# Kernel optimization log

Measured on AMD Instinct MI355X. Metric: run time of the kernel, lower is better.

## Reference

```python
import jax, jax.numpy as jnp
import numpy as np

N_EMBD = 384
HEAD_SIZE = 64
B, T = 16, 2048


def setup_inputs() -> dict:
    key = jax.random.key(0)
    ks = jax.random.split(key, 7)
    s = 1.0 / np.sqrt(N_EMBD)
    return {
        "x": jax.random.normal(ks[0], (B, T, N_EMBD), dtype=jnp.float32),
        "Wq": jax.random.uniform(ks[1], (N_EMBD, HEAD_SIZE), jnp.float32, -s, s),
        "bq": jax.random.uniform(ks[2], (HEAD_SIZE,), jnp.float32, -s, s),
        "Wk": jax.random.uniform(ks[3], (N_EMBD, HEAD_SIZE), jnp.float32, -s, s),
        "bk": jax.random.uniform(ks[4], (HEAD_SIZE,), jnp.float32, -s, s),
        "Wv": jax.random.uniform(ks[5], (N_EMBD, HEAD_SIZE), jnp.float32, -s, s),
        "bv": jax.random.uniform(ks[6], (HEAD_SIZE,), jnp.float32, -s, s),
    }


def reference(x, Wq, bq, Wk, bk, Wv, bv):
    # QKV projections: [B,T,C] @ [C,H] -> [B,T,H]
    q = x @ Wq + bq
    k = x @ Wk + bk
    v = x @ Wv + bv
    scale = k.shape[-1] ** (-0.5)
    # NOTE: original forward applies NO causal mask (tril buffer unused).
    scores = jnp.einsum("bqh,bkh->bqk", q, k) * scale  # [B,T,T]
    wmap = jax.nn.softmax(scores, axis=-1)
    # dropout is identity in eval mode
    out = jnp.einsum("bqk,bkh->bqh", wmap, v)  # [B,T,H]
    return out
```

## Files before the change

kernel.cpp:

```cpp
#include <hip/hip_runtime.h>
#include <hip/hip_bf16.h>
#include <cstdint>

typedef unsigned short u16;
typedef __attribute__((ext_vector_type(8))) short short8;
typedef __attribute__((ext_vector_type(4))) short short4v;
typedef __attribute__((ext_vector_type(4))) float f32x4;

#define MFMA16(a, b, c) __builtin_amdgcn_mfma_f32_16x16x32_bf16((a), (b), (c), 0, 0, 0)

constexpr int Bn   = 16;
constexpr int Tn   = 2048;
constexpr int Cn   = 384;
constexpr int Hn   = 64;
constexpr int XPAD = 392;
constexpr int WPAD = 72;
constexpr long NTOK = (long)Bn * Tn;
constexpr long NELT = NTOK * Hn;

#define QSCALE 0.18033688011112042f

__device__ __forceinline__ u16 f2bf(float f) {
  union { float f; uint32_t u; } c; c.f = f;
  uint32_t u = c.u;
  return (u16)((u + 0x7fffu + ((u >> 16) & 1u)) >> 16);
}

__device__ __forceinline__ uint32_t pkbf(float a, float b) {
  uint32_t d;
  asm("v_cvt_pk_bf16_f32 %0, %1, %2" : "=v"(d) : "v"(a), "v"(b));
  return d;
}

__device__ __forceinline__ void gl16(const u16* g, const u16* l) {
  __builtin_amdgcn_global_load_lds(
      (const __attribute__((address_space(1))) void*)g,
      (__attribute__((address_space(3))) void*)l, 16, 0, 0);
}

__global__ __launch_bounds__(256) void qkv_proj(
    const float* __restrict__ x,
    const float* __restrict__ Wq, const float* __restrict__ bq,
    const float* __restrict__ Wk, const float* __restrict__ bk,
    const float* __restrict__ Wv, const float* __restrict__ bv,
    u16* __restrict__ oq, u16* __restrict__ ok, u16* __restrict__ ovt)
{
  __shared__ u16 xs[64 * XPAD];
  __shared__ u16 wt[3][Hn * WPAD];

  const int t    = threadIdx.x;
  const int lane = t & 63;
  const int w    = t >> 6;
  const int l15  = lane & 15;
  const int lh   = lane >> 4;
  const long r0  = (long)blockIdx.x * 64;

  #pragma unroll
  for (int i = 0; i < 24; ++i) {
    int f4  = t + i * 256;
    int row = f4 / 96, col4 = f4 % 96;
    const float4 xv = *reinterpret_cast<const float4*>(x + (r0 + row) * Cn + col4 * 4);
    u16* p = &xs[row * XPAD + col4 * 4];
    p[0] = f2bf(xv.x); p[1] = f2bf(xv.y); p[2] = f2bf(xv.z); p[3] = f2bf(xv.w);
  }

  const float* Ws[3] = {Wq, Wk, Wv};

  f32x4 acc[3][4];
  #pragma unroll
  for (int m = 0; m < 3; ++m)
    #pragma unroll
    for (int n = 0; n < 4; ++n) acc[m][n] = f32x4{0.f, 0.f, 0.f, 0.f};

  const int hh  = t & 63;
  const int kk0 = (t >> 6) * 16;

  for (int kc = 0; kc < 6; ++kc) {
    __syncthreads();
    #pragma unroll
    for (int m = 0; m < 3; ++m) {
      const float* Wp = Ws[m] + (size_t)(kc * 64 + kk0) * Hn + hh;
      union { short8 s; u16 u[8]; } p0, p1;
      #pragma unroll
      for (int j = 0; j < 8; ++j) p0.u[j] = f2bf(Wp[j * Hn]);
      #pragma unroll
      for (int j = 0; j < 8; ++j) p1.u[j] = f2bf(Wp[(8 + j) * Hn]);
      *reinterpret_cast<short8*>(&wt[m][hh * WPAD + kk0])     = p0.s;
      *reinterpret_cast<short8*>(&wt[m][hh * WPAD + kk0 + 8]) = p1.s;
    }
    __syncthreads();

    #pragma unroll
    for (int ks = 0; ks < 2; ++ks) {
      const short8 a = *reinterpret_cast<const short8*>(
          &xs[(w * 16 + l15) * XPAD + kc * 64 + ks * 32 + lh * 8]);
      #pragma unroll
      for (int m = 0; m < 3; ++m)
        #pragma unroll
        for (int n = 0; n < 4; ++n) {
          const short8 bfr = *reinterpret_cast<const short8*>(
              &wt[m][(n * 16 + l15) * WPAD + ks * 32 + lh * 8]);
          acc[m][n] = MFMA16(a, bfr, acc[m][n]);
        }
    }
  }

  {
    const float* bias[2] = {bq, bk};
    u16*         dst[2]  = {oq, ok};
    const float  scl[2]  = {QSCALE, 1.0f};
    #pragma unroll
    for (int m = 0; m < 2; ++m) {
      #pragma unroll
      for (int n = 0; n < 4; ++n) {
        int col = n * 16 + l15;
        float bb = bias[m][col];
        #pragma unroll
        for (int r = 0; r < 4; ++r) {
          int row = lh * 4 + r;
          dst[m][(r0 + w * 16 + row) * Hn + col] = f2bf((acc[m][n][r] + bb) * scl[m]);
        }
      }
    }
  }
  {
    const long g    = r0 + w * 16 + lh * 4;
    const long bidx = g >> 11;
    const long tloc = g & 2047;
    #pragma unroll
    for (int n = 0; n < 4; ++n) {
      int col = n * 16 + l15;
      float bb = bv[col];
      short4v pk;
      #pragma unroll
      for (int r = 0; r < 4; ++r) pk[r] = (short)f2bf(acc[2][n][r] + bb);
      *reinterpret_cast<short4v*>(ovt + (bidx * Hn + col) * Tn + tloc) = pk;
    }
  }
}

__global__ __launch_bounds__(256) void flash_attn(
    const u16* __restrict__ q, const u16* __restrict__ k,
    const u16* __restrict__ vt, float* __restrict__ opart,
    float* __restrict__ lpart)
{
  __shared__ u16 kbuf[2][64 * 64];
  __shared__ u16 vbuf[2][64 * 64];

  const int t    = threadIdx.x;
  const int lane = t & 63;
  const int w    = t >> 6;
  const int l15  = lane & 15;
  const int lh   = lane >> 4;
  const int swz_id = ((blockIdx.x & 7) << 7) | (blockIdx.x >> 3);
  const int qt    = swz_id & 31;
  const int split = (swz_id >> 5) & 1;
  const int b     = swz_id >> 6;
  const long rowbase = (long)b * Tn + qt * 64;
  const int it0 = split * 16, it1 = it0 + 16;

  short8 aq[2];
  {
    const u16* qrow = q + (rowbase + w * 16 + l15) * Hn;
    aq[0] = *reinterpret_cast<const short8*>(qrow + lh * 8);
    aq[1] = *reinterpret_cast<const short8*>(qrow + 32 + lh * 8);
  }

  f32x4 o[4];
  #pragma unroll
  for (int m = 0; m < 4; ++m) o[m] = f32x4{0.f, 0.f, 0.f, 0.f};
  float lacc = 0.f;

  const u16* kb_g = k  + (long)b * Tn * Hn;
  const u16* vb_g = vt + (long)b * Hn * Tn;

  const int g0 = t, g1 = 256 + t;
  const int r0g = g0 >> 3, c0g = g0 & 7;
  const int r1g = g1 >> 3, c1g = g1 & 7;
  const int ksrc0 = r0g * Hn + ((c0g ^ (r0g & 7)) << 3);
  const int ksrc1 = r1g * Hn + ((c1g ^ (r1g & 7)) << 3);
  const int wb0 = w * 64 * 8;
  const int wb1 = wb0 + 256 * 8;

  const int vrow = w * 16 + (lane >> 2);
  const int vc   = lane & 3;
  const long vgbase = (long)vrow * Tn + vc * 16;
  const int vs_ = vrow & 7;

  const int swz  = l15 & 7;
  const int cks0 = ((0 * 4 + lh) ^ swz) << 3;
  const int cks1 = ((1 * 4 + lh) ^ swz) << 3;
  const int rfr  = l15 * 64;

  int cur = 0;

  {
    const u16* kt = kb_g + (long)it0 * 64 * Hn;
    gl16(kt + ksrc0, &kbuf[0][wb0]);
    gl16(kt + ksrc1, &kbuf[0][wb1]);
    const short8 v0 = *reinterpret_cast<const short8*>(vb_g + vgbase + it0 * 64);
    const short8 v1 = *reinterpret_cast<const short8*>(vb_g + vgbase + it0 * 64 + 8);
    u16* vdst = &vbuf[0][0] + vrow * 64;
    const int gb = (vc >> 1) * 4, off8 = (vc & 1) * 4;
    *reinterpret_cast<short4v*>(vdst + (((gb + 0) ^ vs_) << 3) + off8) = short4v{v0[0], v0[1], v0[2], v0[3]};
    *reinterpret_cast<short4v*>(vdst + (((gb + 1) ^ vs_) << 3) + off8) = short4v{v0[4], v0[5], v0[6], v0[7]};
    *reinterpret_cast<short4v*>(vdst + (((gb + 2) ^ vs_) << 3) + off8) = short4v{v1[0], v1[1], v1[2], v1[3]};
    *reinterpret_cast<short4v*>(vdst + (((gb + 3) ^ vs_) << 3) + off8) = short4v{v1[4], v1[5], v1[6], v1[7]};
  }
  __syncthreads();

  for (int it = it0; it < it1; ++it) {
    short8 nv0, nv1;
    const bool pf = (it + 1 < it1);
    if (pf) {
      const u16* kt = kb_g + (long)(it + 1) * 64 * Hn;
      gl16(kt + ksrc0, &kbuf[cur ^ 1][wb0]);
      gl16(kt + ksrc1, &kbuf[cur ^ 1][wb1]);
      nv0 = *reinterpret_cast<const short8*>(vb_g + vgbase + (it + 1) * 64);
      nv1 = *reinterpret_cast<const short8*>(vb_g + vgbase + (it + 1) * 64 + 8);
    }

    const u16* kc  = &kbuf[cur][0];
    const u16* vcb = &vbuf[cur][0];

    f32x4 s[4];
    #pragma unroll
    for (int n = 0; n < 4; ++n) s[n] = f32x4{0.f, 0.f, 0.f, 0.f};
    #pragma unroll
    for (int n = 0; n < 4; ++n) {
      const short8 ak0 = *reinterpret_cast<const short8*>(&kc[n * 1024 + rfr + cks0]);
      s[n] = MFMA16(ak0, aq[0], s[n]);
      const short8 ak1 = *reinterpret_cast<const short8*>(&kc[n * 1024 + rfr + cks1]);
      s[n] = MFMA16(ak1, aq[1], s[n]);
    }

    #pragma unroll
    for (int n = 0; n < 4; ++n)
      #pragma unroll
      for (int r = 0; r < 4; ++r)
        s[n][r] = __builtin_amdgcn_exp2f(s[n][r]);

    {
      float t0 = (s[0][0] + s[0][1]) + (s[0][2] + s[0][3]);
      float t1 = (s[1][0] + s[1][1]) + (s[1][2] + s[1][3]);
      float t2 = (s[2][0] + s[2][1]) + (s[2][2] + s[2][3]);
      float t3 = (s[3][0] + s[3][1]) + (s[3][2] + s[3][3]);
      lacc += (t0 + t1) + (t2 + t3);
    }

    union { short8 s8; uint32_t u[4]; } B0, B1;
    B0.u[0] = pkbf(s[0][0], s[0][1]); B0.u[1] = pkbf(s[0][2], s[0][3]);
    B0.u[2] = pkbf(s[1][0], s[1][1]); B0.u[3] = pkbf(s[1][2], s[1][3]);
    B1.u[0] = pkbf(s[2][0], s[2][1]); B1.u[1] = pkbf(s[2][2], s[2][3]);
    B1.u[2] = pkbf(s[3][0], s[3][1]); B1.u[3] = pkbf(s[3][2], s[3][3]);

    #pragma unroll
    for (int m = 0; m < 4; ++m) {
      const short8 av0 = *reinterpret_cast<const short8*>(&vcb[m * 1024 + rfr + cks0]);
      o[m] = MFMA16(av0, B0.s8, o[m]);
      const short8 av1 = *reinterpret_cast<const short8*>(&vcb[m * 1024 + rfr + cks1]);
      o[m] = MFMA16(av1, B1.s8, o[m]);
    }

    if (pf) {
      u16* vdst = &vbuf[cur ^ 1][0] + vrow * 64;
      const int gb = (vc >> 1) * 4, off8 = (vc & 1) * 4;
      *reinterpret_cast<short4v*>(vdst + (((gb + 0) ^ vs_) << 3) + off8) = short4v{nv0[0], nv0[1], nv0[2], nv0[3]};
      *reinterpret_cast<short4v*>(vdst + (((gb + 1) ^ vs_) << 3) + off8) = short4v{nv0[4], nv0[5], nv0[6], nv0[7]};
      *reinterpret_cast<short4v*>(vdst + (((gb + 2) ^ vs_) << 3) + off8) = short4v{nv1[0], nv1[1], nv1[2], nv1[3]};
      *reinterpret_cast<short4v*>(vdst + (((gb + 3) ^ vs_) << 3) + off8) = short4v{nv1[4], nv1[5], nv1[6], nv1[7]};
    }

    __syncthreads();
    cur ^= 1;
  }

  float tot = lacc;
  tot += __shfl_xor(tot, 16);
  tot += __shfl_xor(tot, 32);
  const long qrow = rowbase + w * 16 + l15;
  float* od = opart + ((long)split * NELT) + qrow * Hn;
  #pragma unroll
  for (int m = 0; m < 4; ++m) {
    float4 vv;
    vv.x = o[m][0]; vv.y = o[m][1]; vv.z = o[m][2]; vv.w = o[m][3];
    *reinterpret_cast<float4*>(od + m * 16 + lh * 4) = vv;
  }
  if (lh == 0) lpart[(long)split * NTOK + qrow] = tot;
}

__global__ __launch_bounds__(256) void combine(
    const float* __restrict__ op, const float* __restrict__ lp,
    float* __restrict__ out)
{
  const long idx  = (long)blockIdx.x * 256 + threadIdx.x;
  const long base = idx * 4;
  const long row  = base >> 6;
  const float4 a = *reinterpret_cast<const float4*>(op + base);
  const float4 c = *reinterpret_cast<const float4*>(op + NELT + base);
  const float linv = 1.0f / (lp[row] + lp[NTOK + row]);
  float4 r;
  r.x = (a.x + c.x) * linv; r.y = (a.y + c.y) * linv;
  r.z = (a.z + c.z) * linv; r.w = (a.w + c.w) * linv;
  *reinterpret_cast<float4*>(out + base) = r;
}

extern "C" void kernel_launch(void* const* d_in, const int* in_sizes, int n_in,
                              void* d_out, int out_size, void* d_ws, size_t ws_size,
                              hipStream_t stream) {
  const float* x  = (const float*)d_in[0];
  const float* Wq = (const float*)d_in[1];
  const float* bq = (const float*)d_in[2];
  const float* Wk = (const float*)d_in[3];
  const float* bk = (const float*)d_in[4];
  const float* Wv = (const float*)d_in[5];
  const float* bv = (const float*)d_in[6];
  float* out = (float*)d_out;

  u16* qs = (u16*)d_ws;
  u16* ks = qs + NELT;
  u16* vs = ks + NELT;
  float* op = (float*)(vs + NELT);
  float* lp = op + 2 * NELT;

  hipLaunchKernelGGL(qkv_proj, dim3((int)(NTOK / 64)), dim3(256), 0, stream,
                     x, Wq, bq, Wk, bk, Wv, bv, qs, ks, vs);
  hipLaunchKernelGGL(flash_attn, dim3(1024), dim3(256), 0, stream,
                     qs, ks, vs, op, lp);
  hipLaunchKernelGGL(combine, dim3((int)(NELT / 4 / 256)), dim3(256), 0, stream,
                     op, lp, out);
}
```

Baseline: 59.37 us.

## Pre-transpose weights, use single-wave QKV blocks, and split KV four ways

Adds a small kernel that converts and transposes the three weight matrices to bf16 once per call. The projection kernel becomes one wave per 16 rows and reads x and the transposed weights directly from global memory, with no shared-memory staging and no barriers. The attention kernel splits the key range into four parts instead of two, doubling the block count, and the combine kernel sums all four partials. This trades more partial-output traffic and an extra launch for higher parallelism and less per-block LDS work.

```diff
diff --git a/kernel.cpp b/kernel.cpp
--- a/kernel.cpp
+++ b/kernel.cpp
@@ -13,10 +13,10 @@
 constexpr int Tn   = 2048;
 constexpr int Cn   = 384;
 constexpr int Hn   = 64;
-constexpr int XPAD = 392;
-constexpr int WPAD = 72;
 constexpr long NTOK = (long)Bn * Tn;
 constexpr long NELT = NTOK * Hn;
+constexpr int SPLITS = 4;
+constexpr int NT_PER = 32 / SPLITS;
 
 #define QSCALE 0.18033688011112042f
 
@@ -38,33 +38,50 @@
       (__attribute__((address_space(3))) void*)l, 16, 0, 0);
 }
 
-__global__ __launch_bounds__(256) void qkv_proj(
-    const float* __restrict__ x,
-    const float* __restrict__ Wq, const float* __restrict__ bq,
-    const float* __restrict__ Wk, const float* __restrict__ bk,
-    const float* __restrict__ Wv, const float* __restrict__ bv,
+__global__ __launch_bounds__(256) void wtrans(
+    const float* __restrict__ Wq, const float* __restrict__ Wk,
+    const float* __restrict__ Wv, u16* __restrict__ wtd)
+{
+  __shared__ u16 tile[64][65];
+  const int m  = blockIdx.x / 6;
+  const int kc = blockIdx.x % 6;
+  const float* W = (m == 0) ? Wq : (m == 1) ? Wk : Wv;
+  const int t = threadIdx.x;
+
+  {
+    const int kr = t >> 2, seg = t & 3;
+    const float* src = W + (size_t)(kc * 64 + kr) * Hn + seg * 16;
+    #pragma unroll
+    for (int j = 0; j < 4; ++j) {
+      const float4 f = *reinterpret_cast<const float4*>(src + j * 4);
+      u16* p = &tile[kr][seg * 16 + j * 4];
+      p[0] = f2bf(f.x); p[1] = f2bf(f.y); p[2] = f2bf(f.z); p[3] = f2bf(f.w);
+    }
+  }
+  __syncthreads();
+  {
+    const int hr = t >> 2, seg = t & 3;
+    union { short8 s; u16 u[8]; } o0, o1;
+    #pragma unroll
+    for (int j = 0; j < 8; ++j) o0.u[j] = tile[seg * 16 + j][hr];
+    #pragma unroll
+    for (int j = 0; j < 8; ++j) o1.u[j] = tile[seg * 16 + 8 + j][hr];
+    u16* dst = wtd + ((size_t)m * 64 + hr) * Cn + kc * 64 + seg * 16;
+    *reinterpret_cast<short8*>(dst)     = o0.s;
+    *reinterpret_cast<short8*>(dst + 8) = o1.s;
+  }
+}
+
+__global__ __launch_bounds__(64) void qkv_proj(
+    const float* __restrict__ x, const u16* __restrict__ wtd,
+    const float* __restrict__ bq, const float* __restrict__ bk,
+    const float* __restrict__ bv,
     u16* __restrict__ oq, u16* __restrict__ ok, u16* __restrict__ ovt)
 {
-  __shared__ u16 xs[64 * XPAD];
-  __shared__ u16 wt[3][Hn * WPAD];
-
-  const int t    = threadIdx.x;
-  const int lane = t & 63;
-  const int w    = t >> 6;
+  const int lane = threadIdx.x;
   const int l15  = lane & 15;
   const int lh   = lane >> 4;
-  const long r0  = (long)blockIdx.x * 64;
-
-  #pragma unroll
-  for (int i = 0; i < 24; ++i) {
-    int f4  = t + i * 256;
-    int row = f4 / 96, col4 = f4 % 96;
-    const float4 xv = *reinterpret_cast<const float4*>(x + (r0 + row) * Cn + col4 * 4);
-    u16* p = &xs[row * XPAD + col4 * 4];
-    p[0] = f2bf(xv.x); p[1] = f2bf(xv.y); p[2] = f2bf(xv.z); p[3] = f2bf(xv.w);
-  }
-
-  const float* Ws[3] = {Wq, Wk, Wv};
+  const long r0  = (long)blockIdx.x * 16;
 
   f32x4 acc[3][4];
   #pragma unroll
@@ -72,37 +89,29 @@
     #pragma unroll
     for (int n = 0; n < 4; ++n) acc[m][n] = f32x4{0.f, 0.f, 0.f, 0.f};
 
-  const int hh  = t & 63;
-  const int kk0 = (t >> 6) * 16;
-
+  const float* xrow = x + (r0 + l15) * Cn;
+
+  #pragma unroll
   for (int kc = 0; kc < 6; ++kc) {
-    __syncthreads();
-    #pragma unroll
-    for (int m = 0; m < 3; ++m) {
-      const float* Wp = Ws[m] + (size_t)(kc * 64 + kk0) * Hn + hh;
-      union { short8 s; u16 u[8]; } p0, p1;
+    union { short8 s8; uint32_t u[4]; } a[2];
+    #pragma unroll
+    for (int ks = 0; ks < 2; ++ks) {
+      const float* p = xrow + kc * 64 + ks * 32 + lh * 8;
+      const float4 f0 = *reinterpret_cast<const float4*>(p);
+      const float4 f1 = *reinterpret_cast<const float4*>(p + 4);
+      a[ks].u[0] = pkbf(f0.x, f0.y); a[ks].u[1] = pkbf(f0.z, f0.w);
+      a[ks].u[2] = pkbf(f1.x, f1.y); a[ks].u[3] = pkbf(f1.z, f1.w);
+    }
+    #pragma unroll
+    for (int m = 0; m < 3; ++m)
       #pragma unroll
-      for (int j = 0; j < 8; ++j) p0.u[j] = f2bf(Wp[j * Hn]);
-      #pragma unroll
-      for (int j = 0; j < 8; ++j) p1.u[j] = f2bf(Wp[(8 + j) * Hn]);
-      *reinterpret_cast<short8*>(&wt[m][hh * WPAD + kk0])     = p0.s;
-      *reinterpret_cast<short8*>(&wt[m][hh * WPAD + kk0 + 8]) = p1.s;
-    }
-    __syncthreads();
-
-    #pragma unroll
-    for (int ks = 0; ks < 2; ++ks) {
-      const short8 a = *reinterpret_cast<const short8*>(
-          &xs[(w * 16 + l15) * XPAD + kc * 64 + ks * 32 + lh * 8]);
-      #pragma unroll
-      for (int m = 0; m < 3; ++m)
-        #pragma unroll
-        for (int n = 0; n < 4; ++n) {
-          const short8 bfr = *reinterpret_cast<const short8*>(
-              &wt[m][(n * 16 + l15) * WPAD + ks * 32 + lh * 8]);
-          acc[m][n] = MFMA16(a, bfr, acc[m][n]);
-        }
-    }
+      for (int n = 0; n < 4; ++n) {
+        const u16* wrow = wtd + ((size_t)m * 64 + n * 16 + l15) * Cn + kc * 64;
+        const short8 b0 = *reinterpret_cast<const short8*>(wrow + lh * 8);
+        acc[m][n] = MFMA16(a[0].s8, b0, acc[m][n]);
+        const short8 b1 = *reinterpret_cast<const short8*>(wrow + 32 + lh * 8);
+        acc[m][n] = MFMA16(a[1].s8, b1, acc[m][n]);
+      }
   }
 
   {
@@ -118,13 +127,13 @@
         #pragma unroll
         for (int r = 0; r < 4; ++r) {
           int row = lh * 4 + r;
-          dst[m][(r0 + w * 16 + row) * Hn + col] = f2bf((acc[m][n][r] + bb) * scl[m]);
+          dst[m][(r0 + row) * Hn + col] = f2bf((acc[m][n][r] + bb) * scl[m]);
         }
       }
     }
   }
   {
-    const long g    = r0 + w * 16 + lh * 4;
+    const long g    = r0 + lh * 4;
     const long bidx = g >> 11;
     const long tloc = g & 2047;
     #pragma unroll
@@ -152,12 +161,12 @@
   const int w    = t >> 6;
   const int l15  = lane & 15;
   const int lh   = lane >> 4;
-  const int swz_id = ((blockIdx.x & 7) << 7) | (blockIdx.x >> 3);
+  const int swz_id = ((blockIdx.x & 7) << 8) | (blockIdx.x >> 3);
   const int qt    = swz_id & 31;
-  const int split = (swz_id >> 5) & 1;
-  const int b     = swz_id >> 6;
+  const int split = (swz_id >> 5) & (SPLITS - 1);
+  const int b     = swz_id >> 7;
   const long rowbase = (long)b * Tn + qt * 64;
-  const int it0 = split * 16, it1 = it0 + 16;
+  const int it0 = split * NT_PER, it1 = it0 + NT_PER;
 
   short8 aq[2];
   {
@@ -296,12 +305,17 @@
   const long idx  = (long)blockIdx.x * 256 + threadIdx.x;
   const long base = idx * 4;
   const long row  = base >> 6;
-  const float4 a = *reinterpret_cast<const float4*>(op + base);
-  const float4 c = *reinterpret_cast<const float4*>(op + NELT + base);
-  const float linv = 1.0f / (lp[row] + lp[NTOK + row]);
+  float4 acc = *reinterpret_cast<const float4*>(op + base);
+  float lsum = lp[row];
+  #pragma unroll
+  for (int s = 1; s < SPLITS; ++s) {
+    const float4 c = *reinterpret_cast<const float4*>(op + s * NELT + base);
+    acc.x += c.x; acc.y += c.y; acc.z += c.z; acc.w += c.w;
+    lsum += lp[s * NTOK + row];
+  }
+  const float linv = 1.0f / lsum;
   float4 r;
-  r.x = (a.x + c.x) * linv; r.y = (a.y + c.y) * linv;
-  r.z = (a.z + c.z) * linv; r.w = (a.w + c.w) * linv;
+  r.x = acc.x * linv; r.y = acc.y * linv; r.z = acc.z * linv; r.w = acc.w * linv;
   *reinterpret_cast<float4*>(out + base) = r;
 }
 
@@ -317,15 +331,19 @@
   const float* bv = (const float*)d_in[6];
   float* out = (float*)d_out;
 
-  u16* qs = (u16*)d_ws;
-  u16* ks = qs + NELT;
-  u16* vs = ks + NELT;
-  float* op = (float*)(vs + NELT);
-  float* lp = op + 2 * NELT;
-
-  hipLaunchKernelGGL(qkv_proj, dim3((int)(NTOK / 64)), dim3(256), 0, stream,
-                     x, Wq, bq, Wk, bk, Wv, bv, qs, ks, vs);
-  hipLaunchKernelGGL(flash_attn, dim3(1024), dim3(256), 0, stream,
+  u16* qs  = (u16*)d_ws;
+  u16* ks  = qs + NELT;
+  u16* vs  = ks + NELT;
+  u16* wtd = vs + NELT;
+  float* op = (float*)(wtd + 3 * 64 * Cn);
+  float* lp = op + (long)SPLITS * NELT;
+
+  const int FLASH_BLOCKS = Bn * 32 * SPLITS;
+
+  hipLaunchKernelGGL(wtrans, dim3(18), dim3(256), 0, stream, Wq, Wk, Wv, wtd);
+  hipLaunchKernelGGL(qkv_proj, dim3((int)(NTOK / 16)), dim3(64), 0, stream,
+                     x, wtd, bq, bk, bv, qs, ks, vs);
+  hipLaunchKernelGGL(flash_attn, dim3(FLASH_BLOCKS), dim3(256), 0, stream,
                      qs, ks, vs, op, lp);
   hipLaunchKernelGGL(combine, dim3((int)(NELT / 4 / 256)), dim3(256), 0, stream,
                      op, lp, out);
```

Result: slower. 86.52 us (+45.7%).
